# Performance work log

Hardware: AMD Instinct MI355X
Metric: run time of the kernel (lower is better)

## Reference

```python
import jax, jax.numpy as jnp
import numpy as np

N_PDE = 4096
SENSOR_RANGE = 0.08
WINDOW = int(SENSOR_RANGE * N_PDE)   # 327
HALF = WINDOW // 2                   # 163
RESIZE_LEN = 20
FREQS = jnp.array([1.0, 2.0, 4.0, 8.0], dtype=jnp.float32)
EPS = 1e-6  # flax GroupNorm default epsilon
U_MAX, V_MAX = 40.0, 1.0
N_AGENTS = 262144


def setup_inputs() -> dict:
    key = jax.random.key(0)
    ks = jax.random.split(key, 16)

    def w(k, shape):
        fan_in = shape[0]
        return (jax.random.normal(k, shape, jnp.float32) / np.float32(np.sqrt(fan_in)))

    return {
        "z_curr": jax.random.normal(ks[0], (N_PDE,), jnp.float32),
        "z_target": jax.random.normal(ks[1], (N_PDE,), jnp.float32),
        "xi_curr": jax.random.uniform(ks[2], (N_AGENTS,), jnp.float32),
        # branch net (features=[256,256]), each layer: Dense + GroupNorm(1 group) + tanh
        "bW0": w(ks[3], (2 * RESIZE_LEN, 256)), "bb0": jnp.zeros((256,), jnp.float32),
        "bs0": jnp.ones((256,), jnp.float32), "bB0": jnp.zeros((256,), jnp.float32),
        "bW1": w(ks[4], (256, 256)), "bb1": jnp.zeros((256,), jnp.float32),
        "bs1": jnp.ones((256,), jnp.float32), "bB1": jnp.zeros((256,), jnp.float32),
        # trunk net: 8 -> 32 -> 32
        "tW0": w(ks[5], (8, 32)), "tb0": jnp.zeros((32,), jnp.float32),
        "tW1": w(ks[6], (32, 32)), "tb1": jnp.zeros((32,), jnp.float32),
        # combined head: (256+32) -> 32, then two 32 -> 1 heads
        "cW": w(ks[7], (256 + 32, 32)), "cb": jnp.zeros((32,), jnp.float32),
        "uW": w(ks[8], (32, 1)), "ub": jnp.zeros((1,), jnp.float32),
        "vW": w(ks[9], (32, 1)), "vb": jnp.zeros((1,), jnp.float32),
    }


def _local_obs(padded_error, xi):
    # per-agent dynamic slice + finite-difference gradient + bilinear resize
    center = (xi * (N_PDE - 1)).astype(jnp.int32) + HALF
    start = center - HALF
    p_err = jax.lax.dynamic_slice(padded_error, (start,), (WINDOW,))
    p_grad = jnp.gradient(p_err)
    p_err = jax.image.resize(p_err, (RESIZE_LEN,), method='bilinear')
    p_grad = jax.image.resize(p_grad, (RESIZE_LEN,), method='bilinear')
    return jnp.concatenate([p_err, p_grad])  # [40]


def _groupnorm1(x, scale, bias):
    # GroupNorm(num_groups=1) applied per-sample over the feature axis
    mu = jnp.mean(x, axis=-1, keepdims=True)
    var = jnp.var(x, axis=-1, keepdims=True)
    return (x - mu) * jax.lax.rsqrt(var + EPS) * scale + bias


def reference(z_curr, z_target, xi_curr,
              bW0, bb0, bs0, bB0, bW1, bb1, bs1, bB1,
              tW0, tb0, tW1, tb1, cW, cb, uW, ub, vW, vb):
    error = z_curr - z_target
    padded = jnp.pad(error, (HALF, HALF), mode='edge')  # [N_PDE + 2*HALF]

    patches = jax.vmap(lambda xi: _local_obs(padded, xi))(xi_curr)  # [A, 40]

    # branch net
    h = jnp.tanh(_groupnorm1(patches @ bW0 + bb0, bs0, bB0))  # [A, 256]
    h = jnp.tanh(_groupnorm1(h @ bW1 + bb1, bs1, bB1))        # [A, 256]

    # trunk net
    angle = xi_curr[:, None] * FREQS * jnp.pi                 # [A, 4]
    enc = jnp.concatenate([jnp.sin(angle), jnp.cos(angle)], axis=-1)  # [A, 8]
    enc = jnp.tanh(enc @ tW0 + tb0)
    enc = jnp.tanh(enc @ tW1 + tb1)                           # [A, 32]

    combined = jnp.concatenate([h, enc], axis=-1)             # [A, 288]
    x = jnp.tanh(combined @ cW + cb)                          # [A, 32]
    u_raw = (x @ uW + ub).squeeze(-1)
    v_raw = (x @ vW + vb).squeeze(-1)
    return (U_MAX * jnp.tanh(u_raw), V_MAX * jnp.tanh(v_raw))
```

## Files before the change

kernel.cpp:

```cpp
#include <hip/hip_runtime.h>

#define NP      4096
#define WINDOW  327
#define HALF    163
#define RL      20
#define NA      262144
#define GN_EPS  1e-6f
#define R       8
#define NBLK    (NP / R)

__device__ __forceinline__ float tanh_fast(float x) {
  float e = __expf(2.0f * x);
  return 1.0f - 2.0f / (e + 1.0f);
}

__device__ __forceinline__ void halfwave_sum2(float& a, float& b) {
#pragma unroll
  for (int m = 1; m < 32; m <<= 1) {
    a += __shfl_xor(a, m, 64);
    b += __shfl_xor(b, m, 64);
  }
}

#define L_ESP   0
#define L_OBS   336
#define L_HBUF  656
#define L_PART  2736
#define L_HCL   10928
#define L_TOT   11216

__global__ __launch_bounds__(256, 2) void dc_table(
    const float* __restrict__ zc,  const float* __restrict__ zt,
    const float* __restrict__ bW0, const float* __restrict__ bb0,
    const float* __restrict__ bs0, const float* __restrict__ bB0,
    const float* __restrict__ bW1, const float* __restrict__ bb1,
    const float* __restrict__ bs1, const float* __restrict__ bB1,
    const float* __restrict__ tW0, const float* __restrict__ tb0,
    const float* __restrict__ tW1, const float* __restrict__ tb1,
    const float* __restrict__ cW,  const float* __restrict__ cb,
    const float* __restrict__ uW,  const float* __restrict__ ub,
    const float* __restrict__ vW,  const float* __restrict__ vb,
    float* __restrict__ tbl)
{
  __shared__ __align__(16) float sm[L_TOT];
  float* espan = sm + L_ESP;
  float* obsT  = sm + L_OBS;
  float* hbuf  = sm + L_HBUF;
  float* part  = sm + L_PART;
  float* hcL   = sm + L_HCL;

  const int tid = threadIdx.x;
  const int w   = tid >> 6;
  const int l   = tid & 63;
  const int s0  = blockIdx.x * R;

  for (int t = tid; t < WINDOW + R - 1; t += 256) {
    int c = s0 - HALF + t;
    c = c < 0 ? 0 : (c > NP - 1 ? NP - 1 : c);
    espan[t] = zc[c] - zt[c];
  }
  __syncthreads();

  {
    const float INV  = (float)WINDOW / (float)RL;
    const float RINV = (float)RL / (float)WINDOW;
    for (int task = tid; task < R * 2 * RL; task += 256) {
      int q = task % (2 * RL);
      int r = task / (2 * RL);
      int qq = (q < RL) ? q : q - RL;
      float xs = ((float)qq + 0.5f) * INV - 0.5f;
      int jlo = (int)ceilf(xs - INV);  if (jlo < 0) jlo = 0;
      int jhi = (int)floorf(xs + INV); if (jhi > WINDOW - 1) jhi = WINDOW - 1;
      const float* p = espan + r;
      float wsum = 0.0f, acc = 0.0f;
      for (int j = jlo; j <= jhi; ++j) {
        float wq = 1.0f - fabsf(xs - (float)j) * RINV;
        float v;
        if (q < RL) {
          v = p[j];
        } else {
          v = (j == 0) ? (p[1] - p[0]) :
              (j == WINDOW - 1) ? (p[WINDOW - 1] - p[WINDOW - 2]) :
              0.5f * (p[j + 1] - p[j - 1]);
        }
        wsum += wq;
        acc  += wq * v;
      }
      obsT[q * 8 + r] = acc / wsum;
    }
  }
  __syncthreads();

  float acc[R][4];

#pragma unroll
  for (int r = 0; r < R; ++r) { acc[r][0]=0.f; acc[r][1]=0.f; acc[r][2]=0.f; acc[r][3]=0.f; }
#pragma unroll 2
  for (int kk = 0; kk < 10; ++kk) {
    int k = w * 10 + kk;
    float4 wt = *(const float4*)&bW0[k * 256 + 4 * l];
    float4 o0 = *(const float4*)&obsT[k * 8];
    float4 o1 = *(const float4*)&obsT[k * 8 + 4];
    const float wv[4] = {wt.x, wt.y, wt.z, wt.w};
    const float ov[8] = {o0.x, o0.y, o0.z, o0.w, o1.x, o1.y, o1.z, o1.w};
#pragma unroll
    for (int r = 0; r < R; ++r)
#pragma unroll
      for (int j = 0; j < 4; ++j) acc[r][j] = fmaf(ov[r], wv[j], acc[r][j]);
  }

  {
#pragma unroll
    for (int r = 0; r < R; ++r)
      *(float4*)&part[w * 2048 + r * 256 + 4 * l] = make_float4(acc[r][0], acc[r][1], acc[r][2], acc[r][3]);
    __syncthreads();
    int rr = tid >> 5, g = tid & 31;
    float val[8];
    {
      float4 b0 = *(const float4*)&bb0[8 * g];
      float4 b1 = *(const float4*)&bb0[8 * g + 4];
      val[0]=b0.x; val[1]=b0.y; val[2]=b0.z; val[3]=b0.w;
      val[4]=b1.x; val[5]=b1.y; val[6]=b1.z; val[7]=b1.w;
    }
#pragma unroll
    for (int w2 = 0; w2 < 4; ++w2) {
      float4 p0 = *(const float4*)&part[w2 * 2048 + rr * 256 + 8 * g];
      float4 p1 = *(const float4*)&part[w2 * 2048 + rr * 256 + 8 * g + 4];
      val[0]+=p0.x; val[1]+=p0.y; val[2]+=p0.z; val[3]+=p0.w;
      val[4]+=p1.x; val[5]+=p1.y; val[6]+=p1.z; val[7]+=p1.w;
    }
    float s = 0.f, q = 0.f;
#pragma unroll
    for (int i = 0; i < 8; ++i) { s += val[i]; q += val[i] * val[i]; }
    halfwave_sum2(s, q);
    float mu  = s * (1.0f / 256.0f);
    float var = fmaxf(q * (1.0f / 256.0f) - mu * mu, 0.0f);
    float rv  = rsqrtf(var + GN_EPS);
    float4 sc0 = *(const float4*)&bs0[8 * g];
    float4 sc1 = *(const float4*)&bs0[8 * g + 4];
    float4 sh0 = *(const float4*)&bB0[8 * g];
    float4 sh1 = *(const float4*)&bB0[8 * g + 4];
    const float sc[8] = {sc0.x,sc0.y,sc0.z,sc0.w,sc1.x,sc1.y,sc1.z,sc1.w};
    const float sh[8] = {sh0.x,sh0.y,sh0.z,sh0.w,sh1.x,sh1.y,sh1.z,sh1.w};
    float h[8];
#pragma unroll
    for (int i = 0; i < 8; ++i) h[i] = tanh_fast((val[i] - mu) * rv * sc[i] + sh[i]);
    *(float4*)&hbuf[rr * 260 + 8 * g]     = make_float4(h[0], h[1], h[2], h[3]);
    *(float4*)&hbuf[rr * 260 + 8 * g + 4] = make_float4(h[4], h[5], h[6], h[7]);
  }
  __syncthreads();

#pragma unroll
  for (int r = 0; r < R; ++r) { acc[r][0]=0.f; acc[r][1]=0.f; acc[r][2]=0.f; acc[r][3]=0.f; }
#pragma unroll 2
  for (int kk = 0; kk < 64; kk += 4) {
    int k0 = w * 64 + kk;
    float4 wt0 = *(const float4*)&bW1[(k0    ) * 256 + 4 * l];
    float4 wt1 = *(const float4*)&bW1[(k0 + 1) * 256 + 4 * l];
    float4 wt2 = *(const float4*)&bW1[(k0 + 2) * 256 + 4 * l];
    float4 wt3 = *(const float4*)&bW1[(k0 + 3) * 256 + 4 * l];
    float4 hr[R];
#pragma unroll
    for (int r = 0; r < R; ++r) hr[r] = *(const float4*)&hbuf[r * 260 + k0];
#pragma unroll
    for (int r = 0; r < R; ++r) {
      const float* hp = (const float*)&hr[r];
      acc[r][0] = fmaf(hp[0], wt0.x, acc[r][0]); acc[r][1] = fmaf(hp[0], wt0.y, acc[r][1]);
      acc[r][2] = fmaf(hp[0], wt0.z, acc[r][2]); acc[r][3] = fmaf(hp[0], wt0.w, acc[r][3]);
      acc[r][0] = fmaf(hp[1], wt1.x, acc[r][0]); acc[r][1] = fmaf(hp[1], wt1.y, acc[r][1]);
      acc[r][2] = fmaf(hp[1], wt1.z, acc[r][2]); acc[r][3] = fmaf(hp[1], wt1.w, acc[r][3]);
      acc[r][0] = fmaf(hp[2], wt2.x, acc[r][0]); acc[r][1] = fmaf(hp[2], wt2.y, acc[r][1]);
      acc[r][2] = fmaf(hp[2], wt2.z, acc[r][2]); acc[r][3] = fmaf(hp[2], wt2.w, acc[r][3]);
      acc[r][0] = fmaf(hp[3], wt3.x, acc[r][0]); acc[r][1] = fmaf(hp[3], wt3.y, acc[r][1]);
      acc[r][2] = fmaf(hp[3], wt3.z, acc[r][2]); acc[r][3] = fmaf(hp[3], wt3.w, acc[r][3]);
    }
  }

  {
#pragma unroll
    for (int r = 0; r < R; ++r)
      *(float4*)&part[w * 2048 + r * 256 + 4 * l] = make_float4(acc[r][0], acc[r][1], acc[r][2], acc[r][3]);
    __syncthreads();
    int rr = tid >> 5, g = tid & 31;
    float val[8];
    {
      float4 b0 = *(const float4*)&bb1[8 * g];
      float4 b1 = *(const float4*)&bb1[8 * g + 4];
      val[0]=b0.x; val[1]=b0.y; val[2]=b0.z; val[3]=b0.w;
      val[4]=b1.x; val[5]=b1.y; val[6]=b1.z; val[7]=b1.w;
    }
#pragma unroll
    for (int w2 = 0; w2 < 4; ++w2) {
      float4 p0 = *(const float4*)&part[w2 * 2048 + rr * 256 + 8 * g];
      float4 p1 = *(const float4*)&part[w2 * 2048 + rr * 256 + 8 * g + 4];
      val[0]+=p0.x; val[1]+=p0.y; val[2]+=p0.z; val[3]+=p0.w;
      val[4]+=p1.x; val[5]+=p1.y; val[6]+=p1.z; val[7]+=p1.w;
    }
    float s = 0.f, q = 0.f;
#pragma unroll
    for (int i = 0; i < 8; ++i) { s += val[i]; q += val[i] * val[i]; }
    halfwave_sum2(s, q);
    float mu  = s * (1.0f / 256.0f);
    float var = fmaxf(q * (1.0f / 256.0f) - mu * mu, 0.0f);
    float rv  = rsqrtf(var + GN_EPS);
    float4 sc0 = *(const float4*)&bs1[8 * g];
    float4 sc1 = *(const float4*)&bs1[8 * g + 4];
    float4 sh0 = *(const float4*)&bB1[8 * g];
    float4 sh1 = *(const float4*)&bB1[8 * g + 4];
    const float sc[8] = {sc0.x,sc0.y,sc0.z,sc0.w,sc1.x,sc1.y,sc1.z,sc1.w};
    const float sh[8] = {sh0.x,sh0.y,sh0.z,sh0.w,sh1.x,sh1.y,sh1.z,sh1.w};
    float h[8];
#pragma unroll
    for (int i = 0; i < 8; ++i) h[i] = tanh_fast((val[i] - mu) * rv * sc[i] + sh[i]);
    *(float4*)&hbuf[rr * 260 + 8 * g]     = make_float4(h[0], h[1], h[2], h[3]);
    *(float4*)&hbuf[rr * 260 + 8 * g + 4] = make_float4(h[4], h[5], h[6], h[7]);
  }
  __syncthreads();

  {
    int r = tid >> 5, c = tid & 31;
    float ga = cb[c];
#pragma unroll 4
    for (int k = 0; k < 256; k += 4) {
      float4 hv = *(const float4*)&hbuf[r * 260 + k];
      ga = fmaf(hv.x, cW[(k    ) * 32 + c], ga);
      ga = fmaf(hv.y, cW[(k + 1) * 32 + c], ga);
      ga = fmaf(hv.z, cW[(k + 2) * 32 + c], ga);
      ga = fmaf(hv.w, cW[(k + 3) * 32 + c], ga);
    }
    hcL[r * 36 + c] = ga;
  }
  __syncthreads();

  if (tid < 128) {
    int v = tid >> 3, sub = tid & 7;
    int r = v >> 1, e = v & 1;
    int jg = s0 + r + e;
    float xe = (float)jg * (1.0f / 4095.0f);
    float enc[8];
#pragma unroll
    for (int k = 0; k < 4; ++k) {
      float fr = (float)(1 << k);
      float a = (xe * fr) * 3.14159265358979f;
      enc[k]     = sinf(a);
      enc[k + 4] = cosf(a);
    }
    int base = (tid & 63) & ~7;

    float t0v[4];
#pragma unroll
    for (int i = 0; i < 4; ++i) {
      int f = 4 * sub + i;
      float a = tb0[f];
#pragma unroll
      for (int k = 0; k < 8; ++k) a = fmaf(enc[k], tW0[k * 32 + f], a);
      t0v[i] = tanh_fast(a);
    }

    float t1v[4];
#pragma unroll
    for (int i = 0; i < 4; ++i) t1v[i] = tb1[4 * sub + i];
#pragma unroll
    for (int j8 = 0; j8 < 8; ++j8) {
#pragma unroll
      for (int i2 = 0; i2 < 4; ++i2) {
        float tv = __shfl(t0v[i2], base + j8, 64);
        int k = 4 * j8 + i2;
#pragma unroll
        for (int i = 0; i < 4; ++i) t1v[i] = fmaf(tv, tW1[k * 32 + 4 * sub + i], t1v[i]);
      }
    }
#pragma unroll
    for (int i = 0; i < 4; ++i) t1v[i] = tanh_fast(t1v[i]);

    float xvv[4];
#pragma unroll
    for (int i = 0; i < 4; ++i) xvv[i] = hcL[r * 36 + 4 * sub + i];
#pragma unroll
    for (int j8 = 0; j8 < 8; ++j8) {
#pragma unroll
      for (int i2 = 0; i2 < 4; ++i2) {
        float tv = __shfl(t1v[i2], base + j8, 64);
        int k = 4 * j8 + i2;
#pragma unroll
        for (int i = 0; i < 4; ++i) xvv[i] = fmaf(tv, cW[(256 + k) * 32 + 4 * sub + i], xvv[i]);
      }
    }
#pragma unroll
    for (int i = 0; i < 4; ++i) xvv[i] = tanh_fast(xvv[i]);

    float up = 0.f, vp = 0.f;
#pragma unroll
    for (int i = 0; i < 4; ++i) {
      up = fmaf(xvv[i], uW[4 * sub + i], up);
      vp = fmaf(xvv[i], vW[4 * sub + i], vp);
    }
#pragma unroll
    for (int m = 1; m < 8; m <<= 1) {
      up += __shfl_xor(up, m, 64);
      vp += __shfl_xor(vp, m, 64);
    }
    if (sub == 0) {
      int s = s0 + r;
      tbl[4 * s + e]     = 40.0f * tanh_fast(up + ub[0]);
      tbl[4 * s + 2 + e] = tanh_fast(vp + vb[0]);
    }
  }
}

__global__ __launch_bounds__(256) void dc_agents(
    const float* __restrict__ xi_curr, const float4* __restrict__ tbl,
    float* __restrict__ out)
{
  int a = blockIdx.x * 256 + threadIdx.x;
  float xi = xi_curr[a];
  float p = xi * 4095.0f;
  int s = (int)p;
  s = s > 4095 ? 4095 : s;
  float t = p - (float)s;
  float4 tb = tbl[s];
  out[a]      = fmaf(t, tb.y - tb.x, tb.x);
  out[NA + a] = fmaf(t, tb.w - tb.z, tb.z);
}

extern "C" void kernel_launch(void* const* d_in, const int* in_sizes, int n_in,
                              void* d_out, int out_size, void* d_ws, size_t ws_size,
                              hipStream_t stream) {
  const float* zc  = (const float*)d_in[0];
  const float* zt  = (const float*)d_in[1];
  const float* xi  = (const float*)d_in[2];
  const float* bW0 = (const float*)d_in[3];
  const float* bb0 = (const float*)d_in[4];
  const float* bs0 = (const float*)d_in[5];
  const float* bB0 = (const float*)d_in[6];
  const float* bW1 = (const float*)d_in[7];
  const float* bb1 = (const float*)d_in[8];
  const float* bs1 = (const float*)d_in[9];
  const float* bB1 = (const float*)d_in[10];
  const float* tW0 = (const float*)d_in[11];
  const float* tb0 = (const float*)d_in[12];
  const float* tW1 = (const float*)d_in[13];
  const float* tb1 = (const float*)d_in[14];
  const float* cW  = (const float*)d_in[15];
  const float* cb  = (const float*)d_in[16];
  const float* uW  = (const float*)d_in[17];
  const float* ub  = (const float*)d_in[18];
  const float* vW  = (const float*)d_in[19];
  const float* vb  = (const float*)d_in[20];

  float* tbl = (float*)d_ws;
  float* out = (float*)d_out;

  dc_table<<<NBLK, 256, 0, stream>>>(zc, zt, bW0, bb0, bs0, bB0,
                                     bW1, bb1, bs1, bB1,
                                     tW0, tb0, tW1, tb1, cW, cb,
                                     uW, ub, vW, vb, tbl);
  dc_agents<<<NA / 256, 256, 0, stream>>>(xi, (const float4*)tbl, out);
}
```

Before: 127.7 us.

## Double table-kernel block to 512 threads with fp16 split-K partials

The table-building kernel now launches 512 threads (8 waves) per block instead of 256. The K dimension of both branch matmuls is split across 8 waves instead of 4, and the cross-wave partial sums are stored in LDS as half2 so the larger partial buffer fits. The GroupNorm epilogue is remapped so each wave owns one row and reduces over all 64 lanes, and the combined-head dot product is split in two halves joined by a shuffle. This shortens the per-thread serial FMA chains and raises parallelism, at the cost of fp16 rounding in the partial sums and an extra barrier.

```diff
diff --git a/kernel.cpp b/kernel.cpp
--- a/kernel.cpp
+++ b/kernel.cpp
@@ -1,4 +1,5 @@
 #include <hip/hip_runtime.h>
+#include <hip/hip_fp16.h>
 
 #define NP      4096
 #define WINDOW  327
@@ -14,9 +15,9 @@
   return 1.0f - 2.0f / (e + 1.0f);
 }
 
-__device__ __forceinline__ void halfwave_sum2(float& a, float& b) {
-#pragma unroll
-  for (int m = 1; m < 32; m <<= 1) {
+__device__ __forceinline__ void wave_sum64_2(float& a, float& b) {
+#pragma unroll
+  for (int m = 1; m < 64; m <<= 1) {
     a += __shfl_xor(a, m, 64);
     b += __shfl_xor(b, m, 64);
   }
@@ -25,11 +26,10 @@
 #define L_ESP   0
 #define L_OBS   336
 #define L_HBUF  656
-#define L_PART  2736
-#define L_HCL   10928
-#define L_TOT   11216
-
-__global__ __launch_bounds__(256, 2) void dc_table(
+#define L_HCL   2736
+#define L_TOTF  3024
+
+__global__ __launch_bounds__(512, 4) void dc_table(
     const float* __restrict__ zc,  const float* __restrict__ zt,
     const float* __restrict__ bW0, const float* __restrict__ bb0,
     const float* __restrict__ bs0, const float* __restrict__ bB0,
@@ -42,19 +42,19 @@
     const float* __restrict__ vW,  const float* __restrict__ vb,
     float* __restrict__ tbl)
 {
-  __shared__ __align__(16) float sm[L_TOT];
-  float* espan = sm + L_ESP;
-  float* obsT  = sm + L_OBS;
-  float* hbuf  = sm + L_HBUF;
-  float* part  = sm + L_PART;
-  float* hcL   = sm + L_HCL;
+  __shared__ __align__(16) float  smf[L_TOTF];
+  __shared__ __align__(16) __half2 part[8 * 8 * 128];
+  float* espan = smf + L_ESP;
+  float* obsT  = smf + L_OBS;
+  float* hbuf  = smf + L_HBUF;
+  float* hcL   = smf + L_HCL;
 
   const int tid = threadIdx.x;
   const int w   = tid >> 6;
   const int l   = tid & 63;
   const int s0  = blockIdx.x * R;
 
-  for (int t = tid; t < WINDOW + R - 1; t += 256) {
+  for (int t = tid; t < WINDOW + R - 1; t += 512) {
     int c = s0 - HALF + t;
     c = c < 0 ? 0 : (c > NP - 1 ? NP - 1 : c);
     espan[t] = zc[c] - zt[c];
@@ -64,7 +64,7 @@
   {
     const float INV  = (float)WINDOW / (float)RL;
     const float RINV = (float)RL / (float)WINDOW;
-    for (int task = tid; task < R * 2 * RL; task += 256) {
+    for (int task = tid; task < R * 2 * RL; task += 512) {
       int q = task % (2 * RL);
       int r = task / (2 * RL);
       int qq = (q < RL) ? q : q - RL;
@@ -95,9 +95,8 @@
 
 #pragma unroll
   for (int r = 0; r < R; ++r) { acc[r][0]=0.f; acc[r][1]=0.f; acc[r][2]=0.f; acc[r][3]=0.f; }
-#pragma unroll 2
-  for (int kk = 0; kk < 10; ++kk) {
-    int k = w * 10 + kk;
+  for (int kk = 0; kk < 5; ++kk) {
+    int k = w * 5 + kk;
     float4 wt = *(const float4*)&bW0[k * 256 + 4 * l];
     float4 o0 = *(const float4*)&obsT[k * 8];
     float4 o1 = *(const float4*)&obsT[k * 8 + 4];
@@ -108,127 +107,111 @@
 #pragma unroll
       for (int j = 0; j < 4; ++j) acc[r][j] = fmaf(ov[r], wv[j], acc[r][j]);
   }
+#pragma unroll
+  for (int r = 0; r < R; ++r) {
+    part[w * 1024 + r * 128 + 2 * l]     = __float22half2_rn(make_float2(acc[r][0], acc[r][1]));
+    part[w * 1024 + r * 128 + 2 * l + 1] = __float22half2_rn(make_float2(acc[r][2], acc[r][3]));
+  }
+  __syncthreads();
 
   {
-#pragma unroll
-    for (int r = 0; r < R; ++r)
-      *(float4*)&part[w * 2048 + r * 256 + 4 * l] = make_float4(acc[r][0], acc[r][1], acc[r][2], acc[r][3]);
-    __syncthreads();
-    int rr = tid >> 5, g = tid & 31;
-    float val[8];
-    {
-      float4 b0 = *(const float4*)&bb0[8 * g];
-      float4 b1 = *(const float4*)&bb0[8 * g + 4];
-      val[0]=b0.x; val[1]=b0.y; val[2]=b0.z; val[3]=b0.w;
-      val[4]=b1.x; val[5]=b1.y; val[6]=b1.z; val[7]=b1.w;
-    }
-#pragma unroll
-    for (int w2 = 0; w2 < 4; ++w2) {
-      float4 p0 = *(const float4*)&part[w2 * 2048 + rr * 256 + 8 * g];
-      float4 p1 = *(const float4*)&part[w2 * 2048 + rr * 256 + 8 * g + 4];
-      val[0]+=p0.x; val[1]+=p0.y; val[2]+=p0.z; val[3]+=p0.w;
-      val[4]+=p1.x; val[5]+=p1.y; val[6]+=p1.z; val[7]+=p1.w;
-    }
-    float s = 0.f, q = 0.f;
-#pragma unroll
-    for (int i = 0; i < 8; ++i) { s += val[i]; q += val[i] * val[i]; }
-    halfwave_sum2(s, q);
+    const int rr = w, g = l;
+    float4 b = *(const float4*)&bb0[4 * g];
+    float v0 = b.x, v1 = b.y, v2 = b.z, v3 = b.w;
+#pragma unroll
+    for (int w2 = 0; w2 < 8; ++w2) {
+      float2 p0 = __half22float2(part[w2 * 1024 + rr * 128 + 2 * g]);
+      float2 p1 = __half22float2(part[w2 * 1024 + rr * 128 + 2 * g + 1]);
+      v0 += p0.x; v1 += p0.y; v2 += p1.x; v3 += p1.y;
+    }
+    float s = v0 + v1 + v2 + v3;
+    float q = v0*v0 + v1*v1 + v2*v2 + v3*v3;
+    wave_sum64_2(s, q);
     float mu  = s * (1.0f / 256.0f);
     float var = fmaxf(q * (1.0f / 256.0f) - mu * mu, 0.0f);
     float rv  = rsqrtf(var + GN_EPS);
-    float4 sc0 = *(const float4*)&bs0[8 * g];
-    float4 sc1 = *(const float4*)&bs0[8 * g + 4];
-    float4 sh0 = *(const float4*)&bB0[8 * g];
-    float4 sh1 = *(const float4*)&bB0[8 * g + 4];
-    const float sc[8] = {sc0.x,sc0.y,sc0.z,sc0.w,sc1.x,sc1.y,sc1.z,sc1.w};
-    const float sh[8] = {sh0.x,sh0.y,sh0.z,sh0.w,sh1.x,sh1.y,sh1.z,sh1.w};
-    float h[8];
-#pragma unroll
-    for (int i = 0; i < 8; ++i) h[i] = tanh_fast((val[i] - mu) * rv * sc[i] + sh[i]);
-    *(float4*)&hbuf[rr * 260 + 8 * g]     = make_float4(h[0], h[1], h[2], h[3]);
-    *(float4*)&hbuf[rr * 260 + 8 * g + 4] = make_float4(h[4], h[5], h[6], h[7]);
+    float4 sc = *(const float4*)&bs0[4 * g];
+    float4 sh = *(const float4*)&bB0[4 * g];
+    float4 h;
+    h.x = tanh_fast((v0 - mu) * rv * sc.x + sh.x);
+    h.y = tanh_fast((v1 - mu) * rv * sc.y + sh.y);
+    h.z = tanh_fast((v2 - mu) * rv * sc.z + sh.z);
+    h.w = tanh_fast((v3 - mu) * rv * sc.w + sh.w);
+    *(float4*)&hbuf[rr * 260 + 4 * g] = h;
   }
   __syncthreads();
 
 #pragma unroll
   for (int r = 0; r < R; ++r) { acc[r][0]=0.f; acc[r][1]=0.f; acc[r][2]=0.f; acc[r][3]=0.f; }
-#pragma unroll 2
-  for (int kk = 0; kk < 64; kk += 4) {
-    int k0 = w * 64 + kk;
+  for (int kk = 0; kk < 32; kk += 4) {
+    int k0 = w * 32 + kk;
     float4 wt0 = *(const float4*)&bW1[(k0    ) * 256 + 4 * l];
     float4 wt1 = *(const float4*)&bW1[(k0 + 1) * 256 + 4 * l];
     float4 wt2 = *(const float4*)&bW1[(k0 + 2) * 256 + 4 * l];
     float4 wt3 = *(const float4*)&bW1[(k0 + 3) * 256 + 4 * l];
-    float4 hr[R];
-#pragma unroll
-    for (int r = 0; r < R; ++r) hr[r] = *(const float4*)&hbuf[r * 260 + k0];
 #pragma unroll
     for (int r = 0; r < R; ++r) {
-      const float* hp = (const float*)&hr[r];
-      acc[r][0] = fmaf(hp[0], wt0.x, acc[r][0]); acc[r][1] = fmaf(hp[0], wt0.y, acc[r][1]);
-      acc[r][2] = fmaf(hp[0], wt0.z, acc[r][2]); acc[r][3] = fmaf(hp[0], wt0.w, acc[r][3]);
-      acc[r][0] = fmaf(hp[1], wt1.x, acc[r][0]); acc[r][1] = fmaf(hp[1], wt1.y, acc[r][1]);
-      acc[r][2] = fmaf(hp[1], wt1.z, acc[r][2]); acc[r][3] = fmaf(hp[1], wt1.w, acc[r][3]);
-      acc[r][0] = fmaf(hp[2], wt2.x, acc[r][0]); acc[r][1] = fmaf(hp[2], wt2.y, acc[r][1]);
-      acc[r][2] = fmaf(hp[2], wt2.z, acc[r][2]); acc[r][3] = fmaf(hp[2], wt2.w, acc[r][3]);
-      acc[r][0] = fmaf(hp[3], wt3.x, acc[r][0]); acc[r][1] = fmaf(hp[3], wt3.y, acc[r][1]);
-      acc[r][2] = fmaf(hp[3], wt3.z, acc[r][2]); acc[r][3] = fmaf(hp[3], wt3.w, acc[r][3]);
-    }
-  }
+      float4 hv = *(const float4*)&hbuf[r * 260 + k0];
+      acc[r][0] = fmaf(hv.x, wt0.x, acc[r][0]); acc[r][1] = fmaf(hv.x, wt0.y, acc[r][1]);
+      acc[r][2] = fmaf(hv.x, wt0.z, acc[r][2]); acc[r][3] = fmaf(hv.x, wt0.w, acc[r][3]);
+      acc[r][0] = fmaf(hv.y, wt1.x, acc[r][0]); acc[r][1] = fmaf(hv.y, wt1.y, acc[r][1]);
+      acc[r][2] = fmaf(hv.y, wt1.z, acc[r][2]); acc[r][3] = fmaf(hv.y, wt1.w, acc[r][3]);
+      acc[r][0] = fmaf(hv.z, wt2.x, acc[r][0]); acc[r][1] = fmaf(hv.z, wt2.y, acc[r][1]);
+      acc[r][2] = fmaf(hv.z, wt2.z, acc[r][2]); acc[r][3] = fmaf(hv.z, wt2.w, acc[r][3]);
+      acc[r][0] = fmaf(hv.w, wt3.x, acc[r][0]); acc[r][1] = fmaf(hv.w, wt3.y, acc[r][1]);
+      acc[r][2] = fmaf(hv.w, wt3.z, acc[r][2]); acc[r][3] = fmaf(hv.w, wt3.w, acc[r][3]);
+    }
+  }
+  __syncthreads();
+#pragma unroll
+  for (int r = 0; r < R; ++r) {
+    part[w * 1024 + r * 128 + 2 * l]     = __float22half2_rn(make_float2(acc[r][0], acc[r][1]));
+    part[w * 1024 + r * 128 + 2 * l + 1] = __float22half2_rn(make_float2(acc[r][2], acc[r][3]));
+  }
+  __syncthreads();
 
   {
-#pragma unroll
-    for (int r = 0; r < R; ++r)
-      *(float4*)&part[w * 2048 + r * 256 + 4 * l] = make_float4(acc[r][0], acc[r][1], acc[r][2], acc[r][3]);
-    __syncthreads();
-    int rr = tid >> 5, g = tid & 31;
-    float val[8];
-    {
-      float4 b0 = *(const float4*)&bb1[8 * g];
-      float4 b1 = *(const float4*)&bb1[8 * g + 4];
-      val[0]=b0.x; val[1]=b0.y; val[2]=b0.z; val[3]=b0.w;
-      val[4]=b1.x; val[5]=b1.y; val[6]=b1.z; val[7]=b1.w;
-    }
-#pragma unroll
-    for (int w2 = 0; w2 < 4; ++w2) {
-      float4 p0 = *(const float4*)&part[w2 * 2048 + rr * 256 + 8 * g];
-      float4 p1 = *(const float4*)&part[w2 * 2048 + rr * 256 + 8 * g + 4];
-      val[0]+=p0.x; val[1]+=p0.y; val[2]+=p0.z; val[3]+=p0.w;
-      val[4]+=p1.x; val[5]+=p1.y; val[6]+=p1.z; val[7]+=p1.w;
-    }
-    float s = 0.f, q = 0.f;
-#pragma unroll
-    for (int i = 0; i < 8; ++i) { s += val[i]; q += val[i] * val[i]; }
-    halfwave_sum2(s, q);
+    const int rr = w, g = l;
+    float4 b = *(const float4*)&bb1[4 * g];
+    float v0 = b.x, v1 = b.y, v2 = b.z, v3 = b.w;
+#pragma unroll
+    for (int w2 = 0; w2 < 8; ++w2) {
+      float2 p0 = __half22float2(part[w2 * 1024 + rr * 128 + 2 * g]);
+      float2 p1 = __half22float2(part[w2 * 1024 + rr * 128 + 2 * g + 1]);
+      v0 += p0.x; v1 += p0.y; v2 += p1.x; v3 += p1.y;
+    }
+    float s = v0 + v1 + v2 + v3;
+    float q = v0*v0 + v1*v1 + v2*v2 + v3*v3;
+    wave_sum64_2(s, q);
     float mu  = s * (1.0f / 256.0f);
     float var = fmaxf(q * (1.0f / 256.0f) - mu * mu, 0.0f);
     float rv  = rsqrtf(var + GN_EPS);
-    float4 sc0 = *(const float4*)&bs1[8 * g];
-    float4 sc1 = *(const float4*)&bs1[8 * g + 4];
-    float4 sh0 = *(const float4*)&bB1[8 * g];
-    float4 sh1 = *(const float4*)&bB1[8 * g + 4];
-    const float sc[8] = {sc0.x,sc0.y,sc0.z,sc0.w,sc1.x,sc1.y,sc1.z,sc1.w};
-    const float sh[8] = {sh0.x,sh0.y,sh0.z,sh0.w,sh1.x,sh1.y,sh1.z,sh1.w};
-    float h[8];
-#pragma unroll
-    for (int i = 0; i < 8; ++i) h[i] = tanh_fast((val[i] - mu) * rv * sc[i] + sh[i]);
-    *(float4*)&hbuf[rr * 260 + 8 * g]     = make_float4(h[0], h[1], h[2], h[3]);
-    *(float4*)&hbuf[rr * 260 + 8 * g + 4] = make_float4(h[4], h[5], h[6], h[7]);
+    float4 sc = *(const float4*)&bs1[4 * g];
+    float4 sh = *(const float4*)&bB1[4 * g];
+    float4 h;
+    h.x = tanh_fast((v0 - mu) * rv * sc.x + sh.x);
+    h.y = tanh_fast((v1 - mu) * rv * sc.y + sh.y);
+    h.z = tanh_fast((v2 - mu) * rv * sc.z + sh.z);
+    h.w = tanh_fast((v3 - mu) * rv * sc.w + sh.w);
+    *(float4*)&hbuf[rr * 260 + 4 * g] = h;
   }
   __syncthreads();
 
   {
-    int r = tid >> 5, c = tid & 31;
-    float ga = cb[c];
+    int r = tid >> 6;
+    int c = l >> 1, kh = l & 1;
+    float ga = (kh == 0) ? cb[c] : 0.0f;
+    int kbase = kh * 128;
 #pragma unroll 4
-    for (int k = 0; k < 256; k += 4) {
-      float4 hv = *(const float4*)&hbuf[r * 260 + k];
-      ga = fmaf(hv.x, cW[(k    ) * 32 + c], ga);
-      ga = fmaf(hv.y, cW[(k + 1) * 32 + c], ga);
-      ga = fmaf(hv.z, cW[(k + 2) * 32 + c], ga);
-      ga = fmaf(hv.w, cW[(k + 3) * 32 + c], ga);
-    }
-    hcL[r * 36 + c] = ga;
+    for (int k = 0; k < 128; k += 4) {
+      float4 hv = *(const float4*)&hbuf[r * 260 + kbase + k];
+      ga = fmaf(hv.x, cW[(kbase + k    ) * 32 + c], ga);
+      ga = fmaf(hv.y, cW[(kbase + k + 1) * 32 + c], ga);
+      ga = fmaf(hv.z, cW[(kbase + k + 2) * 32 + c], ga);
+      ga = fmaf(hv.w, cW[(kbase + k + 3) * 32 + c], ga);
+    }
+    ga += __shfl_xor(ga, 1, 64);
+    if (kh == 0) hcL[r * 36 + c] = ga;
   }
   __syncthreads();
 
@@ -351,7 +334,7 @@
   float* tbl = (float*)d_ws;
   float* out = (float*)d_out;
 
-  dc_table<<<NBLK, 256, 0, stream>>>(zc, zt, bW0, bb0, bs0, bB0,
+  dc_table<<<NBLK, 512, 0, stream>>>(zc, zt, bW0, bb0, bs0, bB0,
                                      bW1, bb1, bs1, bB1,
                                      tW0, tb0, tW1, tb1, cW, cb,
                                      uW, ub, vW, vb, tbl);
```

Result: slower. 136.6 us (+7.0%).
